# Optimization experiments

Measured on AMD Instinct MI355X. Metric: run time of the kernel, lower is better.

Reference implementation:

```python
import jax, jax.numpy as jnp
import numpy as np

N_NODES = 50000
N_EDGES = 800000
IN_CH = 128
HID_CH = 128
OUT_CH = 10
NUM_GRAPHS = 128


def setup_inputs() -> dict:
    key = jax.random.key(0)
    ks = jax.random.split(key, 10)
    x = jax.random.normal(ks[0], (N_NODES, IN_CH), dtype=jnp.float32)
    edge_index = jax.random.randint(ks[1], (2, N_EDGES), 0, N_NODES, dtype=jnp.int64)
    batch = jnp.sort(jax.random.randint(ks[2], (N_NODES,), 0, NUM_GRAPHS, dtype=jnp.int64))
    s1 = 1.0 / np.sqrt(IN_CH)
    s2 = 1.0 / np.sqrt(HID_CH)
    W1 = jax.random.uniform(ks[3], (IN_CH, HID_CH), jnp.float32, -s1, s1)
    b1 = jnp.zeros((HID_CH,), jnp.float32)
    W2 = jax.random.uniform(ks[4], (HID_CH, HID_CH), jnp.float32, -s2, s2)
    b2 = jnp.zeros((HID_CH,), jnp.float32)
    Wc = jax.random.uniform(ks[5], (HID_CH, OUT_CH), jnp.float32, -s2, s2)
    bc = jax.random.uniform(ks[6], (OUT_CH,), jnp.float32, -s2, s2)
    return {"x": x, "edge_index": edge_index, "batch": batch,
            "W1": W1, "b1": b1, "W2": W2, "b2": b2, "Wc": Wc, "bc": bc}


def _gcn_norm(edge_index, num_nodes):
    # add self-loops, compute symmetric normalization deg^-1/2[src]*deg^-1/2[dst]
    loop = jnp.arange(num_nodes, dtype=edge_index.dtype)
    src = jnp.concatenate([edge_index[0], loop])
    dst = jnp.concatenate([edge_index[1], loop])
    deg = jax.ops.segment_sum(jnp.ones_like(dst, dtype=jnp.float32), dst,
                              num_segments=num_nodes)
    dinv = jnp.where(deg > 0, jax.lax.rsqrt(deg), 0.0)
    norm = dinv[src] * dinv[dst]
    return src, dst, norm


def _gcn_conv(h, src, dst, norm, W, b, num_nodes):
    h = h @ W                                    # [N, out]
    msg = h[src] * norm[:, None]                 # [E+N, out] gather + scale
    agg = jax.ops.segment_sum(msg, dst, num_segments=num_nodes)
    return agg + b


def reference(x, edge_index, batch, W1, b1, W2, b2, Wc, bc):
    n = x.shape[0]
    src, dst, norm = _gcn_norm(edge_index, n)
    h = jax.nn.relu(_gcn_conv(x, src, dst, norm, W1, b1, n))
    h = jax.nn.relu(_gcn_conv(h, src, dst, norm, W2, b2, n))
    # global mean pool over graphs
    sums = jax.ops.segment_sum(h, batch, num_segments=NUM_GRAPHS)
    cnts = jax.ops.segment_sum(jnp.ones((n,), jnp.float32), batch,
                               num_segments=NUM_GRAPHS)
    pooled = sums / jnp.maximum(cnts, 1.0)[:, None]
    # dropout is identity in eval mode
    return pooled @ Wc + bc
```

## Files before the change

### kernel.cpp

```cpp
#include <hip/hip_runtime.h>

#define N_NODES 50000
#define N_EDGES 800000
#define CH 128
#define NOUT 10
#define NUM_GRAPHS 128
#define GR 64
#define GEMM_BLOCKS ((N_NODES + GR - 1) / GR)
#define RANGES 4
#define FILL_SEGS 200
#define FILL_CHUNK (N_EDGES / FILL_SEGS)
#define FILL_BLOCKS (FILL_SEGS * RANGES)
#define DST_RANGE (N_NODES / RANGES)
#define DEG_CAP 64

typedef __attribute__((ext_vector_type(8))) short bf16x8;
typedef __attribute__((ext_vector_type(4))) float f32x4;

union FragU { uint4 u; bf16x8 s; };

__device__ __forceinline__ unsigned pack_bf16(float a, float b) {
    unsigned ua = __float_as_uint(a), ub = __float_as_uint(b);
    ua += 0x7fffu + ((ua >> 16) & 1u);
    ub += 0x7fffu + ((ub >> 16) & 1u);
    return (ua >> 16) | (ub & 0xffff0000u);
}

__device__ __forceinline__ unsigned short cvt_bf16(float v) {
    unsigned u = __float_as_uint(v);
    u += 0x7fffu + ((u >> 16) & 1u);
    return (unsigned short)(u >> 16);
}

__global__ __launch_bounds__(256) void k_prep(const float* __restrict__ W1,
                                              const float* __restrict__ W2,
                                              unsigned short* __restrict__ Wb1,
                                              unsigned short* __restrict__ Wb2,
                                              int* __restrict__ fill_pos,
                                              float* __restrict__ psum) {
    if (blockIdx.x < 2) {
        const float* W = blockIdx.x ? W2 : W1;
        unsigned short* Wb = blockIdx.x ? Wb2 : Wb1;
        for (int i = threadIdx.x; i < CH * CH; i += 256) {
            int k = i >> 7, n = i & 127;
            Wb[((((k >> 3) << 7) + n) << 3) + (k & 7)] = cvt_bf16(W[i]);
        }
    } else if (blockIdx.x < 198) {
        int idx = (blockIdx.x - 2) * 256 + threadIdx.x;
        if (idx < N_NODES) fill_pos[idx] = 0;
    } else {
        psum[(blockIdx.x - 198) * 256 + threadIdx.x] = 0.f;
    }
}

template <bool SCALE, bool ABF16>
__device__ __forceinline__ void gemm_body9(const void* __restrict__ X,
                                           const unsigned short* __restrict__ Wb,
                                           unsigned short* __restrict__ Yb,
                                           const int* __restrict__ cnt,
                                           int bid) {
    const int tid = threadIdx.x;
    const int w = tid >> 6;
    const int lane = tid & 63;
    const int m = lane & 15;
    const int quad = lane >> 4;
    const int row0 = bid * GR + w * 16;

    int row_a = row0 + m;
    if (row_a > N_NODES - 1) row_a = N_NODES - 1;

    FragU af[4];
    if (ABF16) {
        const uint4* Xr = (const uint4*)((const unsigned short*)X + (size_t)row_a * CH);
        #pragma unroll
        for (int ks = 0; ks < 4; ++ks) af[ks].u = Xr[ks * 4 + quad];
    } else {
        const float4* Xr = (const float4*)((const float*)X + (size_t)row_a * CH) + quad * 2;
        float4 a[8];
        #pragma unroll
        for (int ks = 0; ks < 4; ++ks) {
            a[ks * 2]     = Xr[ks * 8];
            a[ks * 2 + 1] = Xr[ks * 8 + 1];
        }
        #pragma unroll
        for (int ks = 0; ks < 4; ++ks) {
            af[ks].u.x = pack_bf16(a[ks * 2].x, a[ks * 2].y);
            af[ks].u.y = pack_bf16(a[ks * 2].z, a[ks * 2].w);
            af[ks].u.z = pack_bf16(a[ks * 2 + 1].x, a[ks * 2 + 1].y);
            af[ks].u.w = pack_bf16(a[ks * 2 + 1].z, a[ks * 2 + 1].w);
        }
    }

    f32x4 acc[8];
    #pragma unroll
    for (int ct = 0; ct < 8; ++ct) acc[ct] = (f32x4){0.f, 0.f, 0.f, 0.f};

    const uint4* Wq = (const uint4*)Wb;
    #pragma unroll
    for (int ks = 0; ks < 4; ++ks) {
        const int kg = ks * 4 + quad;
        #pragma unroll
        for (int ct = 0; ct < 8; ++ct) {
            FragU bfu;
            bfu.u = Wq[kg * 128 + m * 8 + ct];
            acc[ct] = __builtin_amdgcn_mfma_f32_16x16x32_bf16(af[ks].s, bfu.s, acc[ct], 0, 0, 0);
        }
    }

    #pragma unroll
    for (int r = 0; r < 4; ++r) {
        int row = row0 + quad * 4 + r;
        if (row < N_NODES) {
            float s = SCALE ? rsqrtf((float)(cnt[row] + 1)) : 1.0f;
            uint4 o;
            o.x = pack_bf16(acc[0][r] * s, acc[1][r] * s);
            o.y = pack_bf16(acc[2][r] * s, acc[3][r] * s);
            o.z = pack_bf16(acc[4][r] * s, acc[5][r] * s);
            o.w = pack_bf16(acc[6][r] * s, acc[7][r] * s);
            *(uint4*)(Yb + (size_t)row * CH + m * 8) = o;
        }
    }
}

__global__ __launch_bounds__(256) void k_gemm_fill(const float* __restrict__ X,
                                                   const unsigned short* __restrict__ Wb,
                                                   unsigned short* __restrict__ Yb,
                                                   const int* __restrict__ src,
                                                   const int* __restrict__ dst,
                                                   int* __restrict__ fill_pos,
                                                   int* __restrict__ csr_src) {
    if (blockIdx.x < GEMM_BLOCKS) {
        gemm_body9<false, false>(X, Wb, Yb, nullptr, blockIdx.x);
    } else {
        const int b = blockIdx.x - GEMM_BLOCKS;
        const int t = (b + (GEMM_BLOCKS & 7)) & 7;
        const int rng = t >> 1;
        const int seg = ((b >> 3) << 1) | (t & 1);
        const int lo = rng * DST_RANGE, hi = lo + DST_RANGE;
        const int base = seg * FILL_CHUNK;

        int4 d4[4], s4[4];
        #pragma unroll
        for (int i = 0; i < 4; ++i) {
            int off = (i * 256 + threadIdx.x) * 4;
            if (off < FILL_CHUNK) {
                d4[i] = *(const int4*)(dst + base + off);
                s4[i] = *(const int4*)(src + base + off);
            }
        }
        #pragma unroll
        for (int i = 0; i < 4; ++i) {
            int off = (i * 256 + threadIdx.x) * 4;
            if (off < FILL_CHUNK) {
                #pragma unroll
                for (int k = 0; k < 4; ++k) {
                    int d = (&d4[i].x)[k];
                    if (d >= lo && d < hi) {
                        int slot = atomicAdd(&fill_pos[d], 1);
                        if (slot < DEG_CAP) csr_src[(d << 6) + slot] = (&s4[i].x)[k];
                    }
                }
            }
        }
    }
}

__global__ __launch_bounds__(256) void k_gemm9b(const unsigned short* __restrict__ Xb,
                                                const unsigned short* __restrict__ Wb,
                                                unsigned short* __restrict__ Yb,
                                                const int* __restrict__ cnt) {
    gemm_body9<true, true>(Xb, Wb, Yb, cnt, blockIdx.x);
}

__device__ __forceinline__ void acc_row(float (&x)[8], uint4 q, float w) {
    #pragma unroll
    for (int t = 0; t < 4; ++t) {
        unsigned r = ((const unsigned*)&q)[t];
        x[2 * t]     = fmaf(w, __uint_as_float(r << 16), x[2 * t]);
        x[2 * t + 1] = fmaf(w, __uint_as_float(r & 0xffff0000u), x[2 * t + 1]);
    }
}

template <bool HAS_W, bool POOL>
__device__ __forceinline__ void gather_body(const unsigned* __restrict__ tb,
                                            const int* __restrict__ csr_src,
                                            const int* __restrict__ cnt,
                                            const float* __restrict__ bias,
                                            unsigned short* __restrict__ hb,
                                            const int* __restrict__ batch,
                                            float* __restrict__ psum) {
    const int wid = threadIdx.x >> 6;
    const int lane = threadIdx.x & 63;
    const int sub = lane >> 4;
    const int cidx = lane & 15;
    const int v = blockIdx.x * 4 + wid;

    int lenc = cnt[v];
    const float dv = rsqrtf((float)(lenc + 1));
    int len = lenc > DEG_CAP ? DEG_CAP : lenc;

    int u_l = 0;
    float w_l = 0.f;
    if (lane < len) {
        u_l = csr_src[(v << 6) + lane];
        if (HAS_W) w_l = rsqrtf((float)(cnt[u_l] + 1));
    }

    const uint4* tbq = (const uint4*)tb;
    float x[8];
    #pragma unroll
    for (int t = 0; t < 8; ++t) x[t] = 0.f;

    const int ng = (len + 3) >> 2;
    for (int g = 0; g < ng; g += 8) {
        uint4 q[8];
        float w[8];
        #pragma unroll
        for (int k = 0; k < 8; ++k) {
            if (g + k < ng) {
                int idx = (g + k) * 4 + sub;
                bool act = idx < len;
                int ic = act ? idx : 0;
                int u = __shfl(u_l, ic);
                w[k] = act ? (HAS_W ? __shfl(w_l, ic) : 1.f) : 0.f;
                q[k] = tbq[(size_t)u * 16 + cidx];
            }
        }
        #pragma unroll
        for (int k = 0; k < 8; ++k)
            if (g + k < ng) acc_row(x, q[k], w[k]);
    }
    {
        uint4 q = tbq[(size_t)v * 16 + cidx];
        float w = (sub == 0) ? (HAS_W ? dv : 1.f) : 0.f;
        acc_row(x, q, w);
    }

    #pragma unroll
    for (int t = 0; t < 8; ++t) {
        x[t] += __shfl_xor(x[t], 16);
        x[t] += __shfl_xor(x[t], 32);
    }

    const float4* b4 = (const float4*)bias;
    float4 b0 = b4[cidx * 2], b1 = b4[cidx * 2 + 1];
    float o[8];
    o[0] = fmaxf(fmaf(dv, x[0], b0.x), 0.f);
    o[1] = fmaxf(fmaf(dv, x[1], b0.y), 0.f);
    o[2] = fmaxf(fmaf(dv, x[2], b0.z), 0.f);
    o[3] = fmaxf(fmaf(dv, x[3], b0.w), 0.f);
    o[4] = fmaxf(fmaf(dv, x[4], b1.x), 0.f);
    o[5] = fmaxf(fmaf(dv, x[5], b1.y), 0.f);
    o[6] = fmaxf(fmaf(dv, x[6], b1.z), 0.f);
    o[7] = fmaxf(fmaf(dv, x[7], b1.w), 0.f);

    if (POOL) {
        __shared__ float sh[4][128];
        __shared__ int sg[4];
        if (lane == 0) sg[wid] = batch[v];
        if (sub == 0) {
            float4* shp = (float4*)&sh[wid][cidx * 8];
            shp[0] = (float4){o[0], o[1], o[2], o[3]};
            shp[1] = (float4){o[4], o[5], o[6], o[7]};
        }
        __syncthreads();
        const int tid = threadIdx.x;
        if (tid < 128) {
            int g0 = sg[0], g1 = sg[1], g2 = sg[2], g3 = sg[3];
            float v0 = sh[0][tid], v1 = sh[1][tid], v2 = sh[2][tid], v3 = sh[3][tid];
            if (g0 == g3) {
                atomicAdd(&psum[g0 * CH + tid], v0 + v1 + v2 + v3);
            } else {
                if (g0 == g1) v1 += v0; else atomicAdd(&psum[g0 * CH + tid], v0);
                if (g1 == g2) v2 += v1; else atomicAdd(&psum[g1 * CH + tid], v1);
                if (g2 == g3) v3 += v2; else atomicAdd(&psum[g2 * CH + tid], v2);
                atomicAdd(&psum[g3 * CH + tid], v3);
            }
        }
    } else {
        if (sub == 0) {
            uint4 ob;
            ob.x = pack_bf16(o[0], o[1]);
            ob.y = pack_bf16(o[2], o[3]);
            ob.z = pack_bf16(o[4], o[5]);
            ob.w = pack_bf16(o[6], o[7]);
            *(uint4*)(hb + (size_t)v * CH + cidx * 8) = ob;
        }
    }
}

__global__ __launch_bounds__(256) void k_gather_hw(const unsigned* __restrict__ tb,
                                                   const int* __restrict__ csr_src,
                                                   const int* __restrict__ cnt,
                                                   const float* __restrict__ b,
                                                   unsigned short* __restrict__ hb) {
    gather_body<true, false>(tb, csr_src, cnt, b, hb, nullptr, nullptr);
}

__global__ __launch_bounds__(256) void k_gather_pool(const unsigned* __restrict__ tb,
                                                     const int* __restrict__ csr_src,
                                                     const int* __restrict__ cnt,
                                                     const float* __restrict__ b,
                                                     const int* __restrict__ batch,
                                                     float* __restrict__ psum) {
    gather_body<false, true>(tb, csr_src, cnt, b, nullptr, batch, psum);
}

__global__ __launch_bounds__(128) void k_classify(const float* __restrict__ psum,
                                                  const int* __restrict__ batch,
                                                  const float* __restrict__ Wc,
                                                  const float* __restrict__ bc,
                                                  float* __restrict__ out) {
    __shared__ float p[CH];
    __shared__ float sinv;
    int g = blockIdx.x;
    int tid = threadIdx.x;
    if (tid == 0) {
        int lo = 0, hi = N_NODES;
        while (lo < hi) { int mid = (lo + hi) >> 1; if (batch[mid] < g) lo = mid + 1; else hi = mid; }
        int start = lo;
        lo = 0; hi = N_NODES;
        while (lo < hi) { int mid = (lo + hi) >> 1; if (batch[mid] < g + 1) lo = mid + 1; else hi = mid; }
        sinv = 1.0f / fmaxf((float)(lo - start), 1.0f);
    }
    __syncthreads();
    p[tid] = psum[g * CH + tid] * sinv;
    __syncthreads();
    if (tid < NOUT) {
        float acc = bc[tid];
        #pragma unroll 4
        for (int k = 0; k < CH; ++k) acc += p[k] * Wc[k * NOUT + tid];
        out[g * NOUT + tid] = acc;
    }
}

extern "C" void kernel_launch(void* const* d_in, const int* in_sizes, int n_in,
                              void* d_out, int out_size, void* d_ws, size_t ws_size,
                              hipStream_t stream) {
    const float* x     = (const float*)d_in[0];
    const int*   ei    = (const int*)d_in[1];
    const int*   batch = (const int*)d_in[2];
    const float* W1    = (const float*)d_in[3];
    const float* b1    = (const float*)d_in[4];
    const float* W2    = (const float*)d_in[5];
    const float* b2    = (const float*)d_in[6];
    const float* Wc    = (const float*)d_in[7];
    const float* bc    = (const float*)d_in[8];
    float* out = (float*)d_out;

    const int* src = ei;
    const int* dst = ei + N_EDGES;

    int*            fill_pos = (int*)d_ws;
    int*            csr_src  = fill_pos + N_NODES;
    unsigned short* wb1      = (unsigned short*)(csr_src + (size_t)N_NODES * DEG_CAP);
    unsigned short* wb2      = wb1 + CH * CH;
    unsigned short* tb       = wb2 + CH * CH;
    unsigned short* hb16     = tb + (size_t)N_NODES * CH;
    float*          psum     = (float*)(hb16 + (size_t)N_NODES * CH);

    k_prep<<<198 + 64, 256, 0, stream>>>(W1, W2, wb1, wb2, fill_pos, psum);

    k_gemm_fill<<<GEMM_BLOCKS + FILL_BLOCKS, 256, 0, stream>>>(
        x, wb1, tb, src, dst, fill_pos, csr_src);

    k_gather_hw<<<N_NODES / 4, 256, 0, stream>>>((unsigned*)tb, csr_src, fill_pos, b1, hb16);

    k_gemm9b<<<GEMM_BLOCKS, 256, 0, stream>>>(hb16, wb2, tb, fill_pos);

    k_gather_pool<<<N_NODES / 4, 256, 0, stream>>>((unsigned*)tb, csr_src, fill_pos, b2,
                                                   batch, psum);

    k_classify<<<NUM_GRAPHS, 128, 0, stream>>>(psum, batch, Wc, bc, out);
}
```

Measured before the change: 261.2 us.

## Fuse layer-2 GEMM into first gather and split edge fill into 8 ranges

Removes the separate layer-2 GEMM kernel and the intermediate bf16 hidden buffer. The first gather kernel now applies bias and ReLU, packs the row, and multiplies it by W2 per node with MFMA, writing the pre-scaled result directly. The aim is to save a launch and a full write and read of the hidden activations. In exchange, each wave reloads all of W2 for a single node and uses only one of the 16 MFMA rows. Separately, the CSR fill now uses 8 destination ranges with a simpler strided loop, which means each edge chunk is read more times.

Result: slower. 412.2 us (+57.8%).

```diff
diff --git a/kernel.cpp b/kernel.cpp
--- a/kernel.cpp
+++ b/kernel.cpp
@@ -7,11 +7,10 @@
 #define NUM_GRAPHS 128
 #define GR 64
 #define GEMM_BLOCKS ((N_NODES + GR - 1) / GR)
-#define RANGES 4
 #define FILL_SEGS 200
 #define FILL_CHUNK (N_EDGES / FILL_SEGS)
-#define FILL_BLOCKS (FILL_SEGS * RANGES)
-#define DST_RANGE (N_NODES / RANGES)
+#define FILL_BLOCKS (FILL_SEGS * 8)
+#define DST_RANGE (N_NODES / 8)
 #define DEG_CAP 64
 
 typedef __attribute__((ext_vector_type(8))) short bf16x8;
@@ -53,12 +52,10 @@
     }
 }
 
-template <bool SCALE, bool ABF16>
-__device__ __forceinline__ void gemm_body9(const void* __restrict__ X,
-                                           const unsigned short* __restrict__ Wb,
-                                           unsigned short* __restrict__ Yb,
-                                           const int* __restrict__ cnt,
-                                           int bid) {
+__device__ __forceinline__ void gemm_body(const float* __restrict__ X,
+                                          const unsigned short* __restrict__ Wb,
+                                          unsigned short* __restrict__ Yb,
+                                          int bid) {
     const int tid = threadIdx.x;
     const int w = tid >> 6;
     const int lane = tid & 63;
@@ -69,26 +66,20 @@
     int row_a = row0 + m;
     if (row_a > N_NODES - 1) row_a = N_NODES - 1;
 
+    const float4* Xr = (const float4*)(X + (size_t)row_a * CH) + quad * 2;
+    float4 a[8];
+    #pragma unroll
+    for (int ks = 0; ks < 4; ++ks) {
+        a[ks * 2]     = Xr[ks * 8];
+        a[ks * 2 + 1] = Xr[ks * 8 + 1];
+    }
     FragU af[4];
-    if (ABF16) {
-        const uint4* Xr = (const uint4*)((const unsigned short*)X + (size_t)row_a * CH);
-        #pragma unroll
-        for (int ks = 0; ks < 4; ++ks) af[ks].u = Xr[ks * 4 + quad];
-    } else {
-        const float4* Xr = (const float4*)((const float*)X + (size_t)row_a * CH) + quad * 2;
-        float4 a[8];
-        #pragma unroll
-        for (int ks = 0; ks < 4; ++ks) {
-            a[ks * 2]     = Xr[ks * 8];
-            a[ks * 2 + 1] = Xr[ks * 8 + 1];
-        }
-        #pragma unroll
-        for (int ks = 0; ks < 4; ++ks) {
-            af[ks].u.x = pack_bf16(a[ks * 2].x, a[ks * 2].y);
-            af[ks].u.y = pack_bf16(a[ks * 2].z, a[ks * 2].w);
-            af[ks].u.z = pack_bf16(a[ks * 2 + 1].x, a[ks * 2 + 1].y);
-            af[ks].u.w = pack_bf16(a[ks * 2 + 1].z, a[ks * 2 + 1].w);
-        }
+    #pragma unroll
+    for (int ks = 0; ks < 4; ++ks) {
+        af[ks].u.x = pack_bf16(a[ks * 2].x, a[ks * 2].y);
+        af[ks].u.y = pack_bf16(a[ks * 2].z, a[ks * 2].w);
+        af[ks].u.z = pack_bf16(a[ks * 2 + 1].x, a[ks * 2 + 1].y);
+        af[ks].u.w = pack_bf16(a[ks * 2 + 1].z, a[ks * 2 + 1].w);
     }
 
     f32x4 acc[8];
@@ -111,12 +102,11 @@
     for (int r = 0; r < 4; ++r) {
         int row = row0 + quad * 4 + r;
         if (row < N_NODES) {
-            float s = SCALE ? rsqrtf((float)(cnt[row] + 1)) : 1.0f;
             uint4 o;
-            o.x = pack_bf16(acc[0][r] * s, acc[1][r] * s);
-            o.y = pack_bf16(acc[2][r] * s, acc[3][r] * s);
-            o.z = pack_bf16(acc[4][r] * s, acc[5][r] * s);
-            o.w = pack_bf16(acc[6][r] * s, acc[7][r] * s);
+            o.x = pack_bf16(acc[0][r], acc[1][r]);
+            o.y = pack_bf16(acc[2][r], acc[3][r]);
+            o.z = pack_bf16(acc[4][r], acc[5][r]);
+            o.w = pack_bf16(acc[6][r], acc[7][r]);
             *(uint4*)(Yb + (size_t)row * CH + m * 8) = o;
         }
     }
@@ -130,46 +120,27 @@
                                                    int* __restrict__ fill_pos,
                                                    int* __restrict__ csr_src) {
     if (blockIdx.x < GEMM_BLOCKS) {
-        gemm_body9<false, false>(X, Wb, Yb, nullptr, blockIdx.x);
+        gemm_body(X, Wb, Yb, blockIdx.x);
     } else {
         const int b = blockIdx.x - GEMM_BLOCKS;
-        const int t = (b + (GEMM_BLOCKS & 7)) & 7;
-        const int rng = t >> 1;
-        const int seg = ((b >> 3) << 1) | (t & 1);
+        const int rng = b & 7;
+        const int seg = b >> 3;
         const int lo = rng * DST_RANGE, hi = lo + DST_RANGE;
         const int base = seg * FILL_CHUNK;
-
-        int4 d4[4], s4[4];
-        #pragma unroll
-        for (int i = 0; i < 4; ++i) {
-            int off = (i * 256 + threadIdx.x) * 4;
-            if (off < FILL_CHUNK) {
-                d4[i] = *(const int4*)(dst + base + off);
-                s4[i] = *(const int4*)(src + base + off);
-            }
-        }
-        #pragma unroll
-        for (int i = 0; i < 4; ++i) {
-            int off = (i * 256 + threadIdx.x) * 4;
-            if (off < FILL_CHUNK) {
-                #pragma unroll
-                for (int k = 0; k < 4; ++k) {
-                    int d = (&d4[i].x)[k];
-                    if (d >= lo && d < hi) {
-                        int slot = atomicAdd(&fill_pos[d], 1);
-                        if (slot < DEG_CAP) csr_src[(d << 6) + slot] = (&s4[i].x)[k];
-                    }
+        for (int it = threadIdx.x * 4; it < FILL_CHUNK; it += 1024) {
+            int e = base + it;
+            int4 d4 = *(const int4*)(dst + e);
+            int4 s4 = *(const int4*)(src + e);
+            #pragma unroll
+            for (int k = 0; k < 4; ++k) {
+                int d = (&d4.x)[k];
+                if (d >= lo && d < hi) {
+                    int slot = atomicAdd(&fill_pos[d], 1);
+                    if (slot < DEG_CAP) csr_src[(d << 6) + slot] = (&s4.x)[k];
                 }
             }
         }
     }
-}
-
-__global__ __launch_bounds__(256) void k_gemm9b(const unsigned short* __restrict__ Xb,
-                                                const unsigned short* __restrict__ Wb,
-                                                unsigned short* __restrict__ Yb,
-                                                const int* __restrict__ cnt) {
-    gemm_body9<true, true>(Xb, Wb, Yb, cnt, blockIdx.x);
 }
 
 __device__ __forceinline__ void acc_row(float (&x)[8], uint4 q, float w) {
@@ -181,14 +152,12 @@
     }
 }
 
-template <bool HAS_W, bool POOL>
-__device__ __forceinline__ void gather_body(const unsigned* __restrict__ tb,
-                                            const int* __restrict__ csr_src,
-                                            const int* __restrict__ cnt,
-                                            const float* __restrict__ bias,
-                                            unsigned short* __restrict__ hb,
-                                            const int* __restrict__ batch,
-                                            float* __restrict__ psum) {
+__global__ __launch_bounds__(256) void k_gather_w2(const unsigned* __restrict__ tb,
+                                                   const int* __restrict__ csr_src,
+                                                   const int* __restrict__ cnt,
+                                                   const float* __restrict__ bias,
+                                                   const unsigned short* __restrict__ Wb,
+                                                   unsigned short* __restrict__ tb2) {
     const int wid = threadIdx.x >> 6;
     const int lane = threadIdx.x & 63;
     const int sub = lane >> 4;
@@ -203,7 +172,7 @@
     float w_l = 0.f;
     if (lane < len) {
         u_l = csr_src[(v << 6) + lane];
-        if (HAS_W) w_l = rsqrtf((float)(cnt[u_l] + 1));
+        w_l = rsqrtf((float)(cnt[u_l] + 1));
     }
 
     const uint4* tbq = (const uint4*)tb;
@@ -222,7 +191,7 @@
                 bool act = idx < len;
                 int ic = act ? idx : 0;
                 int u = __shfl(u_l, ic);
-                w[k] = act ? (HAS_W ? __shfl(w_l, ic) : 1.f) : 0.f;
+                w[k] = act ? __shfl(w_l, ic) : 0.f;
                 q[k] = tbq[(size_t)u * 16 + cidx];
             }
         }
@@ -232,10 +201,104 @@
     }
     {
         uint4 q = tbq[(size_t)v * 16 + cidx];
-        float w = (sub == 0) ? (HAS_W ? dv : 1.f) : 0.f;
+        float w = (sub == 0) ? dv : 0.f;
         acc_row(x, q, w);
     }
-
+    #pragma unroll
+    for (int t = 0; t < 8; ++t) {
+        x[t] += __shfl_xor(x[t], 16);
+        x[t] += __shfl_xor(x[t], 32);
+    }
+
+    const float4* b4 = (const float4*)bias;
+    float4 b0 = b4[cidx * 2], b1v = b4[cidx * 2 + 1];
+    unsigned pk[4];
+    pk[0] = pack_bf16(fmaxf(fmaf(dv, x[0], b0.x), 0.f),
+                      fmaxf(fmaf(dv, x[1], b0.y), 0.f));
+    pk[1] = pack_bf16(fmaxf(fmaf(dv, x[2], b0.z), 0.f),
+                      fmaxf(fmaf(dv, x[3], b0.w), 0.f));
+    pk[2] = pack_bf16(fmaxf(fmaf(dv, x[4], b1v.x), 0.f),
+                      fmaxf(fmaf(dv, x[5], b1v.y), 0.f));
+    pk[3] = pack_bf16(fmaxf(fmaf(dv, x[6], b1v.z), 0.f),
+                      fmaxf(fmaf(dv, x[7], b1v.w), 0.f));
+
+    f32x4 acc[8];
+    #pragma unroll
+    for (int ct = 0; ct < 8; ++ct) acc[ct] = (f32x4){0.f, 0.f, 0.f, 0.f};
+    const uint4* Wq = (const uint4*)Wb;
+    #pragma unroll
+    for (int ks = 0; ks < 4; ++ks) {
+        const int hl = ks * 4 + sub;
+        FragU af;
+        af.u.x = __shfl(pk[0], hl);
+        af.u.y = __shfl(pk[1], hl);
+        af.u.z = __shfl(pk[2], hl);
+        af.u.w = __shfl(pk[3], hl);
+        #pragma unroll
+        for (int ct = 0; ct < 8; ++ct) {
+            FragU bfu;
+            bfu.u = Wq[hl * 128 + cidx * 8 + ct];
+            acc[ct] = __builtin_amdgcn_mfma_f32_16x16x32_bf16(af.s, bfu.s, acc[ct], 0, 0, 0);
+        }
+    }
+    if (sub == 0) {
+        uint4 o;
+        o.x = pack_bf16(acc[0][0] * dv, acc[1][0] * dv);
+        o.y = pack_bf16(acc[2][0] * dv, acc[3][0] * dv);
+        o.z = pack_bf16(acc[4][0] * dv, acc[5][0] * dv);
+        o.w = pack_bf16(acc[6][0] * dv, acc[7][0] * dv);
+        *(uint4*)(tb2 + (size_t)v * CH + cidx * 8) = o;
+    }
+}
+
+__global__ __launch_bounds__(256) void k_gather_pool(const unsigned* __restrict__ tb,
+                                                     const int* __restrict__ csr_src,
+                                                     const int* __restrict__ cnt,
+                                                     const float* __restrict__ bias,
+                                                     const int* __restrict__ batch,
+                                                     float* __restrict__ psum) {
+    const int wid = threadIdx.x >> 6;
+    const int lane = threadIdx.x & 63;
+    const int sub = lane >> 4;
+    const int cidx = lane & 15;
+    const int v = blockIdx.x * 4 + wid;
+
+    int lenc = cnt[v];
+    const float dv = rsqrtf((float)(lenc + 1));
+    int len = lenc > DEG_CAP ? DEG_CAP : lenc;
+
+    int u_l = 0;
+    if (lane < len) u_l = csr_src[(v << 6) + lane];
+
+    const uint4* tbq = (const uint4*)tb;
+    float x[8];
+    #pragma unroll
+    for (int t = 0; t < 8; ++t) x[t] = 0.f;
+
+    const int ng = (len + 3) >> 2;
+    for (int g = 0; g < ng; g += 8) {
+        uint4 q[8];
+        float w[8];
+        #pragma unroll
+        for (int k = 0; k < 8; ++k) {
+            if (g + k < ng) {
+                int idx = (g + k) * 4 + sub;
+                bool act = idx < len;
+                int ic = act ? idx : 0;
+                int u = __shfl(u_l, ic);
+                w[k] = act ? 1.f : 0.f;
+                q[k] = tbq[(size_t)u * 16 + cidx];
+            }
+        }
+        #pragma unroll
+        for (int k = 0; k < 8; ++k)
+            if (g + k < ng) acc_row(x, q[k], w[k]);
+    }
+    {
+        uint4 q = tbq[(size_t)v * 16 + cidx];
+        float w = (sub == 0) ? 1.f : 0.f;
+        acc_row(x, q, w);
+    }
     #pragma unroll
     for (int t = 0; t < 8; ++t) {
         x[t] += __shfl_xor(x[t], 16);
@@ -254,56 +317,28 @@
     o[6] = fmaxf(fmaf(dv, x[6], b1.z), 0.f);
     o[7] = fmaxf(fmaf(dv, x[7], b1.w), 0.f);
 
-    if (POOL) {
-        __shared__ float sh[4][128];
-        __shared__ int sg[4];
-        if (lane == 0) sg[wid] = batch[v];
-        if (sub == 0) {
-            float4* shp = (float4*)&sh[wid][cidx * 8];
-            shp[0] = (float4){o[0], o[1], o[2], o[3]};
-            shp[1] = (float4){o[4], o[5], o[6], o[7]};
-        }
-        __syncthreads();
-        const int tid = threadIdx.x;
-        if (tid < 128) {
-            int g0 = sg[0], g1 = sg[1], g2 = sg[2], g3 = sg[3];
-            float v0 = sh[0][tid], v1 = sh[1][tid], v2 = sh[2][tid], v3 = sh[3][tid];
-            if (g0 == g3) {
-                atomicAdd(&psum[g0 * CH + tid], v0 + v1 + v2 + v3);
-            } else {
-                if (g0 == g1) v1 += v0; else atomicAdd(&psum[g0 * CH + tid], v0);
-                if (g1 == g2) v2 += v1; else atomicAdd(&psum[g1 * CH + tid], v1);
-                if (g2 == g3) v3 += v2; else atomicAdd(&psum[g2 * CH + tid], v2);
-                atomicAdd(&psum[g3 * CH + tid], v3);
-            }
-        }
-    } else {
-        if (sub == 0) {
-            uint4 ob;
-            ob.x = pack_bf16(o[0], o[1]);
-            ob.y = pack_bf16(o[2], o[3]);
-            ob.z = pack_bf16(o[4], o[5]);
-            ob.w = pack_bf16(o[6], o[7]);
-            *(uint4*)(hb + (size_t)v * CH + cidx * 8) = ob;
-        }
-    }
-}
-
-__global__ __launch_bounds__(256) void k_gather_hw(const unsigned* __restrict__ tb,
-                                                   const int* __restrict__ csr_src,
-                                                   const int* __restrict__ cnt,
-                                                   const float* __restrict__ b,
-                                                   unsigned short* __restrict__ hb) {
-    gather_body<true, false>(tb, csr_src, cnt, b, hb, nullptr, nullptr);
-}
-
-__global__ __launch_bounds__(256) void k_gather_pool(const unsigned* __restrict__ tb,
-                                                     const int* __restrict__ csr_src,
-                                                     const int* __restrict__ cnt,
-                                                     const float* __restrict__ b,
-                                                     const int* __restrict__ batch,
-                                                     float* __restrict__ psum) {
-    gather_body<false, true>(tb, csr_src, cnt, b, nullptr, batch, psum);
+    __shared__ float sh[4][128];
+    __shared__ int sg[4];
+    if (lane == 0) sg[wid] = batch[v];
+    if (sub == 0) {
+        float4* shp = (float4*)&sh[wid][cidx * 8];
+        shp[0] = (float4){o[0], o[1], o[2], o[3]};
+        shp[1] = (float4){o[4], o[5], o[6], o[7]};
+    }
+    __syncthreads();
+    const int tid = threadIdx.x;
+    if (tid < 128) {
+        int g0 = sg[0], g1 = sg[1], g2 = sg[2], g3 = sg[3];
+        float v0 = sh[0][tid], v1 = sh[1][tid], v2 = sh[2][tid], v3 = sh[3][tid];
+        if (g0 == g3) {
+            atomicAdd(&psum[g0 * CH + tid], v0 + v1 + v2 + v3);
+        } else {
+            if (g0 == g1) v1 += v0; else atomicAdd(&psum[g0 * CH + tid], v0);
+            if (g1 == g2) v2 += v1; else atomicAdd(&psum[g1 * CH + tid], v1);
+            if (g2 == g3) v3 += v2; else atomicAdd(&psum[g2 * CH + tid], v2);
+            atomicAdd(&psum[g3 * CH + tid], v3);
+        }
+    }
 }
 
 __global__ __launch_bounds__(128) void k_classify(const float* __restrict__ psum,
@@ -356,19 +391,18 @@
     unsigned short* wb1      = (unsigned short*)(csr_src + (size_t)N_NODES * DEG_CAP);
     unsigned short* wb2      = wb1 + CH * CH;
     unsigned short* tb       = wb2 + CH * CH;
-    unsigned short* hb16     = tb + (size_t)N_NODES * CH;
-    float*          psum     = (float*)(hb16 + (size_t)N_NODES * CH);
+    unsigned short* tb2      = tb + (size_t)N_NODES * CH;
+    float*          psum     = (float*)(tb2 + (size_t)N_NODES * CH);
 
     k_prep<<<198 + 64, 256, 0, stream>>>(W1, W2, wb1, wb2, fill_pos, psum);
 
     k_gemm_fill<<<GEMM_BLOCKS + FILL_BLOCKS, 256, 0, stream>>>(
         x, wb1, tb, src, dst, fill_pos, csr_src);
 
-    k_gather_hw<<<N_NODES / 4, 256, 0, stream>>>((unsigned*)tb, csr_src, fill_pos, b1, hb16);
-
-    k_gemm9b<<<GEMM_BLOCKS, 256, 0, stream>>>(hb16, wb2, tb, fill_pos);
-
-    k_gather_pool<<<N_NODES / 4, 256, 0, stream>>>((unsigned*)tb, csr_src, fill_pos, b2,
+    k_gather_w2<<<N_NODES / 4, 256, 0, stream>>>((unsigned*)tb, csr_src, fill_pos, b1,
+                                                 wb2, tb2);
+
+    k_gather_pool<<<N_NODES / 4, 256, 0, stream>>>((unsigned*)tb2, csr_src, fill_pos, b2,
                                                    batch, psum);
 
     k_classify<<<NUM_GRAPHS, 128, 0, stream>>>(psum, batch, Wc, bc, out);
```
